# Optimization experiments

Hardware: AMD Instinct MI355X
Metric: run time of the kernel (lower is better)

Reference implementation:

```python
import jax, jax.numpy as jnp
import numpy as np

B, L, D = 2, 2048, 1024
H, G = 16, 2            # num_heads, num_kv_groups
HPG = H // G            # heads per kv group = 8
DQK, DV = 128, 128      # qk_head_dim, v_head_dim (head_dim=64, ratios=2.0)


def setup_inputs() -> dict:
    key = jax.random.key(0)
    ks = jax.random.split(key, 12)

    def xavier(k, shape, scale=1.0):
        fan_in, fan_out = shape[0], shape[1]
        lim = np.sqrt(6.0 / (fan_in + fan_out))
        return jax.random.uniform(k, shape, jnp.float32, -lim, lim) * scale

    return {
        "in_q": jax.random.normal(ks[0], (B, L, D), jnp.float32),
        "in_k": jax.random.normal(ks[1], (B, L, D), jnp.float32),
        "in_v": jax.random.normal(ks[2], (B, L, D), jnp.float32),
        # weights stored as [in, out] (transpose of torch Linear); qk_init_scale=0.5
        "Wq": xavier(ks[3], (D, H * DQK), 0.5),
        "bq": jnp.zeros((H * DQK,), jnp.float32),
        "Wk": xavier(ks[4], (D, G * DQK), 0.5),
        "bk": jnp.zeros((G * DQK,), jnp.float32),
        "Wv": xavier(ks[5], (D, G * DV)),
        "bv": jnp.zeros((G * DV,), jnp.float32),
        "Wo": xavier(ks[6], (H * DV, D)),
        "bo": jnp.zeros((D,), jnp.float32),
        "q_extra_scale": jnp.ones((1,), jnp.float32),
    }


def reference(in_q, in_k, in_v, Wq, bq, Wk, bk, Wv, bv, Wo, bo, q_extra_scale):
    # fused projections
    q = (in_q @ Wq + bq) * q_extra_scale              # [B,L,H*DQK]
    k = in_k @ Wk + bk                                 # [B,L,G*DQK]
    v = in_v @ Wv + bv                                 # [B,L,G*DV]

    # reshape: keep GQA group structure instead of materializing repeat_interleave
    q = q.reshape(B, L, G, HPG, DQK)                   # heads grouped: head h = g*HPG + m
    k = k.reshape(B, L, G, DQK)
    v = v.reshape(B, L, G, DV)

    scale = 1.0 / np.sqrt(DQK)
    # scores: [B,G,HPG,L_q,L_kv]
    scores = jnp.einsum("bsgmd,btgd->bgmst", q, k) * scale
    causal = jnp.tril(jnp.ones((L, L), bool))          # is_causal=True
    scores = jnp.where(causal, scores, jnp.finfo(scores.dtype).min)
    attn = jax.nn.softmax(scores, axis=-1)
    ctx = jnp.einsum("bgmst,btgd->bsgmd", attn, v)     # [B,L,G,HPG,DV]
    ctx = ctx.reshape(B, L, H * DV)
    return ctx @ Wo + bo                               # [B,L,D]
```

## Files before the change

kernel.cpp:

```cpp
#include <hip/hip_runtime.h>


typedef __bf16 bf16;
typedef __bf16 bf16x8 __attribute__((ext_vector_type(8)));
typedef __bf16 bf16x4 __attribute__((ext_vector_type(4)));
typedef float f32x4 __attribute__((ext_vector_type(4)));
typedef float float4v __attribute__((ext_vector_type(4)));

#define MFMA_BF16(a, b, c) __builtin_amdgcn_mfma_f32_16x16x32_bf16((a), (b), (c), 0, 0, 0)

static constexpr int Bz = 2, Lz = 2048, Dz = 1024;
static constexpr int Hz = 16, Gz = 2;
static constexpr int DQKz = 128, DVz = 128;

__device__ __forceinline__ void async_copy16(const bf16* g, bf16* l) {
    __builtin_amdgcn_global_load_lds(
        (const __attribute__((address_space(1))) unsigned int*)g,
        (__attribute__((address_space(3))) unsigned int*)l, 16, 0, 0);
}

__global__ __launch_bounds__(256) void prep(
    const float* __restrict__ q, const float* __restrict__ k,
    const float* __restrict__ v, bf16* __restrict__ dq,
    bf16* __restrict__ dk, bf16* __restrict__ dv,
    const float* __restrict__ Wq, const float* __restrict__ Wk,
    const float* __restrict__ Wv, const float* __restrict__ Wo,
    bf16* __restrict__ WqT, bf16* __restrict__ WkT,
    bf16* __restrict__ WvT, bf16* __restrict__ WoT)
{
    int bid = blockIdx.x;
    if (bid < 6144) {
        const float* s = bid < 2048 ? q : (bid < 4096 ? k : v);
        bf16* d = bid < 2048 ? dq : (bid < 4096 ? dk : dv);
        int i = (bid & 2047) * 2048 + threadIdx.x * 8;
        float4v a = *(const float4v*)(s + i);
        float4v b = *(const float4v*)(s + i + 4);
        bf16x8 o;
        #pragma unroll
        for (int j = 0; j < 4; ++j) { o[j] = (bf16)a[j]; o[j + 4] = (bf16)b[j]; }
        *(bf16x8*)(d + i) = o;
        return;
    }
    bid -= 6144;
    const float* W; bf16* WT; int K, N;
    if (bid < 2048)      { W = Wq; WT = WqT; K = 1024; N = 2048; }
    else if (bid < 2304) { W = Wk; WT = WkT; K = 1024; N = 256;  bid -= 2048; }
    else if (bid < 2560) { W = Wv; WT = WvT; K = 1024; N = 256;  bid -= 2304; }
    else                 { W = Wo; WT = WoT; K = 2048; N = 1024; bid -= 2560; }
    int tiles_n = N >> 5;
    int n0 = (bid % tiles_n) * 32, k0 = (bid / tiles_n) * 32;

    __shared__ bf16 t[32][33];
    int tx = threadIdx.x & 31, ty = threadIdx.x >> 5;
    #pragma unroll
    for (int i = 0; i < 4; ++i)
        t[ty + i * 8][tx] = (bf16)W[(size_t)(k0 + ty + i * 8) * N + n0 + tx];
    __syncthreads();
    #pragma unroll
    for (int i = 0; i < 4; ++i)
        WT[(size_t)(n0 + ty + i * 8) * K + k0 + tx] = t[tx][ty + i * 8];
}

template <typename TC>
__device__ __forceinline__ void gemm_tile(
    const bf16* __restrict__ A, const bf16* __restrict__ BT,
    const float* __restrict__ bias, float scale, TC* __restrict__ C,
    int M, int N, int K, int m0, int n0, bool trans_out,
    bf16 (&As)[2][128 * 64], bf16 (&Bs)[2][128 * 64])
{
    const int tid  = threadIdx.x;
    const int wave = tid >> 6;
    const int lane = tid & 63;
    const int quad = lane >> 4;
    const int l16  = lane & 15;
    const int sw   = l16 & 7;
    const int wm = wave >> 2, wn = wave & 3;

    f32x4 acc[4][2] = {};

    auto stage = [&](int k0, int buf) {
        #pragma unroll
        for (int s = 0; s < 2; ++s) {
            int i = s * 512 + tid;
            int row = i >> 3, c = (i & 7) ^ (row & 7);
            async_copy16(A + (size_t)(m0 + row) * K + k0 + c * 8, &As[buf][i * 8]);
        }
        #pragma unroll
        for (int s = 0; s < 2; ++s) {
            int i = s * 512 + tid;
            int row = i >> 3, c = (i & 7) ^ (row & 7);
            async_copy16(BT + (size_t)(n0 + row) * K + k0 + c * 8, &Bs[buf][i * 8]);
        }
    };

    stage(0, 0);
    int cur = 0;
    for (int k0 = 0; k0 < K; k0 += 64) {
        __syncthreads();
        if (k0 + 64 < K) stage(k0 + 64, cur ^ 1);

        #pragma unroll
        for (int ks = 0; ks < 2; ++ks) {
            bf16x8 af[4], bfv[2];
            #pragma unroll
            for (int mt = 0; mt < 4; ++mt)
                af[mt] = *(const bf16x8*)(&As[cur][((wm * 64 + mt * 16 + l16) * 8
                                                    + ((ks * 4 + quad) ^ sw)) * 8]);
            #pragma unroll
            for (int nt = 0; nt < 2; ++nt)
                bfv[nt] = *(const bf16x8*)(&Bs[cur][((wn * 32 + nt * 16 + l16) * 8
                                                     + ((ks * 4 + quad) ^ sw)) * 8]);
            #pragma unroll
            for (int mt = 0; mt < 4; ++mt)
                #pragma unroll
                for (int nt = 0; nt < 2; ++nt)
                    acc[mt][nt] = MFMA_BF16(af[mt], bfv[nt], acc[mt][nt]);
        }
        cur ^= 1;
    }

    #pragma unroll
    for (int nt = 0; nt < 2; ++nt) {
        int col = n0 + wn * 32 + nt * 16 + l16;
        float bv = bias[col];
        #pragma unroll
        for (int mt = 0; mt < 4; ++mt) {
            int row = m0 + wm * 64 + mt * 16 + quad * 4;
            if (trans_out) {
                struct V4 { TC v[4]; } o;
                #pragma unroll
                for (int r = 0; r < 4; ++r)
                    o.v[r] = (TC)((acc[mt][nt][r] + bv) * scale);
                *(V4*)(&C[(size_t)col * M + row]) = o;
            } else {
                #pragma unroll
                for (int r = 0; r < 4; ++r)
                    C[(size_t)(row + r) * N + col] =
                        (TC)((acc[mt][nt][r] + bv) * scale);
            }
        }
    }
}

__global__ __launch_bounds__(512, 4) void proj_qkv(
    const bf16* __restrict__ aq, const bf16* __restrict__ ak,
    const bf16* __restrict__ av, const bf16* __restrict__ WqT,
    const bf16* __restrict__ WkT, const bf16* __restrict__ WvT,
    const float* __restrict__ bq, const float* __restrict__ bk,
    const float* __restrict__ bv, const float* __restrict__ qsc,
    bf16* __restrict__ Qw, bf16* __restrict__ Kw, bf16* __restrict__ VwT)
{
    __shared__ bf16 As[2][128 * 64];
    __shared__ bf16 Bs[2][128 * 64];
    int bid = blockIdx.x;
    if (bid < 512) {
        float scale = qsc[0] * 0.08838834764831845f * 1.4426950408889634f;
        gemm_tile<bf16>(aq, WqT, bq, scale, Qw, 4096, 2048, 1024,
                        (bid >> 4) * 128, (bid & 15) * 128, false, As, Bs);
    } else if (bid < 576) {
        int b2 = bid - 512;
        gemm_tile<bf16>(ak, WkT, bk, 1.0f, Kw, 4096, 256, 1024,
                        (b2 >> 1) * 128, (b2 & 1) * 128, false, As, Bs);
    } else {
        int b2 = bid - 576;
        gemm_tile<bf16>(av, WvT, bv, 1.0f, VwT, 4096, 256, 1024,
                        (b2 >> 1) * 128, (b2 & 1) * 128, true, As, Bs);
    }
}

__global__ __launch_bounds__(512, 4) void proj_o(
    const bf16* __restrict__ Cw, const bf16* __restrict__ WoT,
    const float* __restrict__ bo, float* __restrict__ out)
{
    __shared__ bf16 As[2][128 * 64];
    __shared__ bf16 Bs[2][128 * 64];
    gemm_tile<float>(Cw, WoT, bo, 1.0f, out, 4096, 1024, 2048,
                     (blockIdx.x >> 3) * 128, (blockIdx.x & 7) * 128,
                     false, As, Bs);
}

__global__ __launch_bounds__(256, 2) void attn_fused(
    const bf16* __restrict__ Q,
    const bf16* __restrict__ Kp,
    const bf16* __restrict__ VT,
    bf16* __restrict__ ctx)
{
    __shared__ bf16 Kb[2][64 * 128];
    __shared__ bf16 Vb[2][128 * 64];
    __shared__ bf16 Ps[4][16 * 72];

    const int tid  = threadIdx.x;
    const int wave = tid >> 6;
    const int lane = tid & 63;
    const int quad = lane >> 4;
    const int l16  = lane & 15;
    const int sw   = l16 & 7;

    const int h = blockIdx.y;
    const int b = blockIdx.z;
    const int g = h >> 3;

    const bf16* kgbase = Kp + (size_t)(b * Lz) * (Gz * DQKz) + g * DQKz;
    const bf16* vgbase = VT + (size_t)(g * DVz) * (Bz * Lz) + b * Lz;

    auto stage = [&](int kt, int buf) {
        const bf16* kb = kgbase + (size_t)(kt * 64) * (Gz * DQKz);
        #pragma unroll
        for (int s = 0; s < 4; ++s) {
            int i = s * 256 + tid;
            int key = i >> 4, c = (i & 15) ^ (key & 7);
            async_copy16(kb + (size_t)key * (Gz * DQKz) + c * 8, &Kb[buf][i * 8]);
        }
        const bf16* vb = vgbase + kt * 64;
        #pragma unroll
        for (int s = 0; s < 4; ++s) {
            int i = s * 256 + tid;
            int dv = i >> 3, c = (i & 7) ^ (dv & 7);
            async_copy16(vb + (size_t)dv * (Bz * Lz) + c * 8, &Vb[buf][i * 8]);
        }
    };

    for (int pass = 0; pass < 2; ++pass) {
        const int qt  = pass == 0 ? (31 - blockIdx.x) : blockIdx.x;
        const int q0  = qt * 64;
        const int nkt = qt + 1;
        const int qrow = q0 + wave * 16 + l16;

        bf16x8 qf[4];
        {
            const bf16* qbase = Q + (size_t)(b * Lz + qrow) * (Hz * DQKz) + h * DQKz;
            #pragma unroll
            for (int ks = 0; ks < 4; ++ks)
                qf[ks] = *(const bf16x8*)(qbase + ks * 32 + quad * 8);
        }

        f32x4 oacc[8] = {};
        float lsum = 0.0f;

        if (pass) __syncthreads();
        stage(0, 0);
        int cur = 0;

        bf16* ps = Ps[wave];

        for (int kt = 0; kt < nkt; ++kt) {
            __syncthreads();
            if (kt + 1 < nkt) stage(kt + 1, cur ^ 1);

            const bf16* kcur = Kb[cur];
            const bf16* vcur = Vb[cur];

            f32x4 sacc[4] = {};
            #pragma unroll
            for (int nf = 0; nf < 4; ++nf) {
                #pragma unroll
                for (int ks = 0; ks < 4; ++ks) {
                    bf16x8 kf = *(const bf16x8*)(&kcur[((nf * 16 + l16) * 16
                                                        + ((ks * 4 + quad) ^ sw)) * 8]);
                    sacc[nf] = MFMA_BF16(kf, qf[ks], sacc[nf]);
                }
            }

            float pv[4][4];
            if (kt == nkt - 1) {
                const int kv0 = kt * 64;
                #pragma unroll
                for (int nf = 0; nf < 4; ++nf) {
                    int keyb = kv0 + nf * 16 + quad * 4;
                    #pragma unroll
                    for (int r = 0; r < 4; ++r)
                        pv[nf][r] = (keyb + r > qrow) ? 0.0f
                                                      : exp2f(sacc[nf][r] - 8.0f);
                }
            } else {
                #pragma unroll
                for (int nf = 0; nf < 4; ++nf)
                    #pragma unroll
                    for (int r = 0; r < 4; ++r)
                        pv[nf][r] = exp2f(sacc[nf][r] - 8.0f);
            }

            #pragma unroll
            for (int nf = 0; nf < 4; ++nf)
                lsum += (pv[nf][0] + pv[nf][1]) + (pv[nf][2] + pv[nf][3]);

            #pragma unroll
            for (int nf = 0; nf < 4; ++nf) {
                bf16x4 pk;
                #pragma unroll
                for (int r = 0; r < 4; ++r) pk[r] = (bf16)pv[nf][r];
                *(bf16x4*)(&ps[l16 * 72 + nf * 16 + quad * 4]) = pk;
            }

            #pragma unroll
            for (int ks2 = 0; ks2 < 2; ++ks2) {
                bf16x8 pf = *(const bf16x8*)(&ps[l16 * 72 + ks2 * 32 + quad * 8]);
                #pragma unroll
                for (int nf2 = 0; nf2 < 8; ++nf2) {
                    bf16x8 vf = *(const bf16x8*)(&vcur[((nf2 * 16 + l16) * 8
                                                        + ((ks2 * 4 + quad) ^ sw)) * 8]);
                    oacc[nf2] = MFMA_BF16(vf, pf, oacc[nf2]);
                }
            }
            cur ^= 1;
        }

        lsum += __shfl_xor(lsum, 16);
        lsum += __shfl_xor(lsum, 32);
        const float inv = 1.0f / lsum;

        bf16* cbase = ctx + (size_t)(b * Lz + qrow) * (Hz * DVz) + h * DVz;
        #pragma unroll
        for (int nf2 = 0; nf2 < 8; ++nf2) {
            bf16x4 o4;
            #pragma unroll
            for (int r = 0; r < 4; ++r) o4[r] = (bf16)(oacc[nf2][r] * inv);
            *(bf16x4*)(&cbase[nf2 * 16 + quad * 4]) = o4;
        }
    }
}

extern "C" void kernel_launch(void* const* d_in, const int* in_sizes, int n_in,
                              void* d_out, int out_size, void* d_ws, size_t ws_size,
                              hipStream_t stream)
{
    (void)in_sizes; (void)n_in; (void)out_size; (void)ws_size;

    const float* in_q = (const float*)d_in[0];
    const float* in_k = (const float*)d_in[1];
    const float* in_v = (const float*)d_in[2];
    const float* Wq   = (const float*)d_in[3];
    const float* bq   = (const float*)d_in[4];
    const float* Wk   = (const float*)d_in[5];
    const float* bk   = (const float*)d_in[6];
    const float* Wv   = (const float*)d_in[7];
    const float* bv   = (const float*)d_in[8];
    const float* Wo   = (const float*)d_in[9];
    const float* bo   = (const float*)d_in[10];
    const float* qsc  = (const float*)d_in[11];
    float* out = (float*)d_out;

    const int M = Bz * Lz;
    const int NQ = Hz * DQKz;
    const int NKV = Gz * DQKz;

    bf16* aq  = (bf16*)d_ws;
    bf16* WqT = aq  + (size_t)M * Dz;
    bf16* WkT = WqT + (size_t)NQ * Dz;
    bf16* WvT = WkT + (size_t)NKV * Dz;
    bf16* WoT = WvT + (size_t)NKV * Dz;
    bf16* Qw  = WoT + (size_t)Dz * NQ;
    bf16* Kw  = Qw  + (size_t)M * NQ;
    bf16* VwT = Kw  + (size_t)M * NKV;
    bf16* Cw  = VwT + (size_t)NKV * M;
    bf16* ak  = Cw;
    bf16* av  = Cw + (size_t)M * Dz;

    prep<<<dim3(10752), dim3(256), 0, stream>>>(
        in_q, in_k, in_v, aq, ak, av, Wq, Wk, Wv, Wo, WqT, WkT, WvT, WoT);

    proj_qkv<<<dim3(640), dim3(512), 0, stream>>>(
        aq, ak, av, WqT, WkT, WvT, bq, bk, bv, qsc, Qw, Kw, VwT);

    attn_fused<<<dim3(Lz / 128, Hz, Bz), dim3(256), 0, stream>>>(Qw, Kw, VwT, Cw);

    proj_o<<<dim3(256), dim3(512), 0, stream>>>(Cw, WoT, bo, out);
}
```

Measured before the change: 263.7 us.

## Switch attention to 32x32 MFMA with split-KV waves and register-resident P

Rewrites the attention inner loop to use 32x32x16 bf16 MFMAs, with waves split as 2 query tiles by 2 KV halves. The softmax probabilities are packed with v_cvt_pk_bf16 and rearranged via permlane32_swap, so they stay in registers instead of round-tripping through LDS. The two KV-half partial outputs and row sums are combined through LDS at the end of each pass. Staging and fragment offsets are also precomputed outside the loop, trading extra epilogue synchronisation and register pressure for fewer LDS operations and larger MFMA tiles.

```diff
diff --git a/kernel.cpp b/kernel.cpp
--- a/kernel.cpp
+++ b/kernel.cpp
@@ -5,9 +5,11 @@
 typedef __bf16 bf16x8 __attribute__((ext_vector_type(8)));
 typedef __bf16 bf16x4 __attribute__((ext_vector_type(4)));
 typedef float f32x4 __attribute__((ext_vector_type(4)));
+typedef float f32x16 __attribute__((ext_vector_type(16)));
 typedef float float4v __attribute__((ext_vector_type(4)));
 
 #define MFMA_BF16(a, b, c) __builtin_amdgcn_mfma_f32_16x16x32_bf16((a), (b), (c), 0, 0, 0)
+#define MFMA32(a, b, c)    __builtin_amdgcn_mfma_f32_32x32x16_bf16((a), (b), (c), 0, 0, 0)
 
 static constexpr int Bz = 2, Lz = 2048, Dz = 1024;
 static constexpr int Hz = 16, Gz = 2;
@@ -17,6 +19,12 @@
     __builtin_amdgcn_global_load_lds(
         (const __attribute__((address_space(1))) unsigned int*)g,
         (__attribute__((address_space(3))) unsigned int*)l, 16, 0, 0);
+}
+
+__device__ __forceinline__ unsigned cvt_pk_bf16(float lo, float hi) {
+    unsigned r;
+    asm("v_cvt_pk_bf16_f32 %0, %1, %2" : "=v"(r) : "v"(lo), "v"(hi));
+    return r;
 }
 
 __global__ __launch_bounds__(256) void prep(
@@ -187,14 +195,15 @@
 {
     __shared__ bf16 Kb[2][64 * 128];
     __shared__ bf16 Vb[2][128 * 64];
-    __shared__ bf16 Ps[4][16 * 72];
 
     const int tid  = threadIdx.x;
     const int wave = tid >> 6;
     const int lane = tid & 63;
-    const int quad = lane >> 4;
-    const int l16  = lane & 15;
-    const int sw   = l16 & 7;
+    const int hi   = lane >> 5;
+    const int l31  = lane & 31;
+    const int s7   = l31 & 7;
+    const int wq   = wave >> 1;
+    const int kvw  = wave & 1;
 
     const int h = blockIdx.y;
     const int b = blockIdx.z;
@@ -203,46 +212,58 @@
     const bf16* kgbase = Kp + (size_t)(b * Lz) * (Gz * DQKz) + g * DQKz;
     const bf16* vgbase = VT + (size_t)(g * DVz) * (Bz * Lz) + b * Lz;
 
+    int kgo[4], vgo[4], ldso[4];
+    #pragma unroll
+    for (int s = 0; s < 4; ++s) {
+        int i = s * 256 + tid;
+        ldso[s] = i * 8;
+        int key = i >> 4, ck = (i & 15) ^ (key & 7);
+        kgo[s] = key * (Gz * DQKz) + ck * 8;
+        int dvr = i >> 3, cv = (i & 7) ^ (dvr & 7);
+        vgo[s] = dvr * (Bz * Lz) + cv * 8;
+    }
     auto stage = [&](int kt, int buf) {
         const bf16* kb = kgbase + (size_t)(kt * 64) * (Gz * DQKz);
-        #pragma unroll
-        for (int s = 0; s < 4; ++s) {
-            int i = s * 256 + tid;
-            int key = i >> 4, c = (i & 15) ^ (key & 7);
-            async_copy16(kb + (size_t)key * (Gz * DQKz) + c * 8, &Kb[buf][i * 8]);
-        }
         const bf16* vb = vgbase + kt * 64;
         #pragma unroll
-        for (int s = 0; s < 4; ++s) {
-            int i = s * 256 + tid;
-            int dv = i >> 3, c = (i & 7) ^ (dv & 7);
-            async_copy16(vb + (size_t)dv * (Bz * Lz) + c * 8, &Vb[buf][i * 8]);
-        }
+        for (int s = 0; s < 4; ++s) async_copy16(kb + kgo[s], &Kb[buf][ldso[s]]);
+        #pragma unroll
+        for (int s = 0; s < 4; ++s) async_copy16(vb + vgo[s], &Vb[buf][ldso[s]]);
     };
 
+    int koff[8];
+    #pragma unroll
+    for (int ks = 0; ks < 8; ++ks)
+        koff[ks] = ((kvw * 32 + l31) * 16 + ((ks * 2 + hi) ^ s7)) * 8;
+    int voff[4][2];
+    #pragma unroll
+    for (int dt = 0; dt < 4; ++dt)
+        #pragma unroll
+        for (int kss = 0; kss < 2; ++kss)
+            voff[dt][kss] = ((dt * 32 + l31) * 8
+                             + ((kvw * 4 + kss * 2 + hi) ^ s7)) * 8;
+
     for (int pass = 0; pass < 2; ++pass) {
-        const int qt  = pass == 0 ? (31 - blockIdx.x) : blockIdx.x;
+        const int qt  = pass == 0 ? (31 - (int)blockIdx.x) : (int)blockIdx.x;
         const int q0  = qt * 64;
         const int nkt = qt + 1;
-        const int qrow = q0 + wave * 16 + l16;
-
-        bf16x8 qf[4];
+        const int qrow = q0 + wq * 32 + l31;
+
+        bf16x8 qf[8];
         {
             const bf16* qbase = Q + (size_t)(b * Lz + qrow) * (Hz * DQKz) + h * DQKz;
             #pragma unroll
-            for (int ks = 0; ks < 4; ++ks)
-                qf[ks] = *(const bf16x8*)(qbase + ks * 32 + quad * 8);
-        }
-
-        f32x4 oacc[8] = {};
+            for (int s = 0; s < 8; ++s)
+                qf[s] = *(const bf16x8*)(qbase + s * 16 + hi * 8);
+        }
+
+        f32x16 oacc[4] = {};
         float lsum = 0.0f;
 
         if (pass) __syncthreads();
         stage(0, 0);
         int cur = 0;
 
-        bf16* ps = Ps[wave];
-
         for (int kt = 0; kt < nkt; ++kt) {
             __syncthreads();
             if (kt + 1 < nkt) stage(kt + 1, cur ^ 1);
@@ -250,72 +271,92 @@
             const bf16* kcur = Kb[cur];
             const bf16* vcur = Vb[cur];
 
-            f32x4 sacc[4] = {};
-            #pragma unroll
-            for (int nf = 0; nf < 4; ++nf) {
-                #pragma unroll
-                for (int ks = 0; ks < 4; ++ks) {
-                    bf16x8 kf = *(const bf16x8*)(&kcur[((nf * 16 + l16) * 16
-                                                        + ((ks * 4 + quad) ^ sw)) * 8]);
-                    sacc[nf] = MFMA_BF16(kf, qf[ks], sacc[nf]);
-                }
-            }
-
-            float pv[4][4];
+            f32x16 sacc = {};
+            #pragma unroll
+            for (int ks = 0; ks < 8; ++ks) {
+                bf16x8 kf = *(const bf16x8*)(kcur + koff[ks]);
+                sacc = MFMA32(kf, qf[ks], sacc);
+            }
+
+            float pv[16];
             if (kt == nkt - 1) {
-                const int kv0 = kt * 64;
-                #pragma unroll
-                for (int nf = 0; nf < 4; ++nf) {
-                    int keyb = kv0 + nf * 16 + quad * 4;
-                    #pragma unroll
-                    for (int r = 0; r < 4; ++r)
-                        pv[nf][r] = (keyb + r > qrow) ? 0.0f
-                                                      : exp2f(sacc[nf][r] - 8.0f);
+                #pragma unroll
+                for (int r = 0; r < 16; ++r) {
+                    int key = kvw * 32 + (r & 3) + 8 * (r >> 2) + 4 * hi;
+                    pv[r] = (key > wq * 32 + l31) ? 0.0f
+                                                  : exp2f(sacc[r] - 8.0f);
                 }
             } else {
                 #pragma unroll
-                for (int nf = 0; nf < 4; ++nf)
-                    #pragma unroll
-                    for (int r = 0; r < 4; ++r)
-                        pv[nf][r] = exp2f(sacc[nf][r] - 8.0f);
-            }
-
-            #pragma unroll
-            for (int nf = 0; nf < 4; ++nf)
-                lsum += (pv[nf][0] + pv[nf][1]) + (pv[nf][2] + pv[nf][3]);
-
-            #pragma unroll
-            for (int nf = 0; nf < 4; ++nf) {
-                bf16x4 pk;
-                #pragma unroll
-                for (int r = 0; r < 4; ++r) pk[r] = (bf16)pv[nf][r];
-                *(bf16x4*)(&ps[l16 * 72 + nf * 16 + quad * 4]) = pk;
-            }
-
-            #pragma unroll
-            for (int ks2 = 0; ks2 < 2; ++ks2) {
-                bf16x8 pf = *(const bf16x8*)(&ps[l16 * 72 + ks2 * 32 + quad * 8]);
-                #pragma unroll
-                for (int nf2 = 0; nf2 < 8; ++nf2) {
-                    bf16x8 vf = *(const bf16x8*)(&vcur[((nf2 * 16 + l16) * 8
-                                                        + ((ks2 * 4 + quad) ^ sw)) * 8]);
-                    oacc[nf2] = MFMA_BF16(vf, pf, oacc[nf2]);
-                }
+                for (int r = 0; r < 16; ++r)
+                    pv[r] = exp2f(sacc[r] - 8.0f);
+            }
+            lsum += ((pv[0] + pv[1]) + (pv[2] + pv[3]))
+                  + ((pv[4] + pv[5]) + (pv[6] + pv[7]))
+                  + ((pv[8] + pv[9]) + (pv[10] + pv[11]))
+                  + ((pv[12] + pv[13]) + (pv[14] + pv[15]));
+
+            unsigned c0 = cvt_pk_bf16(pv[0],  pv[1]);
+            unsigned c1 = cvt_pk_bf16(pv[2],  pv[3]);
+            unsigned c2 = cvt_pk_bf16(pv[4],  pv[5]);
+            unsigned c3 = cvt_pk_bf16(pv[6],  pv[7]);
+            unsigned c4 = cvt_pk_bf16(pv[8],  pv[9]);
+            unsigned c5 = cvt_pk_bf16(pv[10], pv[11]);
+            unsigned c6 = cvt_pk_bf16(pv[12], pv[13]);
+            unsigned c7 = cvt_pk_bf16(pv[14], pv[15]);
+            asm("v_permlane32_swap_b32 %0, %1" : "+v"(c0), "+v"(c2));
+            asm("v_permlane32_swap_b32 %0, %1" : "+v"(c1), "+v"(c3));
+            asm("v_permlane32_swap_b32 %0, %1" : "+v"(c4), "+v"(c6));
+            asm("v_permlane32_swap_b32 %0, %1" : "+v"(c5), "+v"(c7));
+            union { unsigned u[4]; bf16x8 v; } p0 = {{c0, c1, c2, c3}};
+            union { unsigned u[4]; bf16x8 v; } p1 = {{c4, c5, c6, c7}};
+
+            #pragma unroll
+            for (int dt = 0; dt < 4; ++dt) {
+                bf16x8 vf0 = *(const bf16x8*)(vcur + voff[dt][0]);
+                oacc[dt] = MFMA32(vf0, p0.v, oacc[dt]);
+                bf16x8 vf1 = *(const bf16x8*)(vcur + voff[dt][1]);
+                oacc[dt] = MFMA32(vf1, p1.v, oacc[dt]);
             }
             cur ^= 1;
         }
 
-        lsum += __shfl_xor(lsum, 16);
         lsum += __shfl_xor(lsum, 32);
+
+        float* E0 = (float*)Kb;
+        float* E1 = (float*)Vb;
+        float* LS = (float*)Vb + 6000;
+        __syncthreads();
+        #pragma unroll
+        for (int t = 0; t < 2; ++t) {
+            int dt = (1 - kvw) * 2 + t;
+            float* E = t ? E1 : E0;
+            #pragma unroll
+            for (int j = 0; j < 4; ++j) {
+                f32x4 v4 = { oacc[dt][4 * j],     oacc[dt][4 * j + 1],
+                             oacc[dt][4 * j + 2], oacc[dt][4 * j + 3] };
+                *(f32x4*)&E[(wave * 64 + lane) * 20 + 4 * j] = v4;
+            }
+        }
+        if (lane < 32) LS[wave * 32 + lane] = lsum;
+        __syncthreads();
+        lsum += LS[(wave ^ 1) * 32 + l31];
         const float inv = 1.0f / lsum;
 
         bf16* cbase = ctx + (size_t)(b * Lz + qrow) * (Hz * DVz) + h * DVz;
         #pragma unroll
-        for (int nf2 = 0; nf2 < 8; ++nf2) {
-            bf16x4 o4;
-            #pragma unroll
-            for (int r = 0; r < 4; ++r) o4[r] = (bf16)(oacc[nf2][r] * inv);
-            *(bf16x4*)(&cbase[nf2 * 16 + quad * 4]) = o4;
+        for (int t = 0; t < 2; ++t) {
+            int dt = kvw * 2 + t;
+            float* E = t ? E1 : E0;
+            #pragma unroll
+            for (int j = 0; j < 4; ++j) {
+                f32x4 p4 = *(const f32x4*)&E[((wave ^ 1) * 64 + lane) * 20 + 4 * j];
+                bf16x4 o4;
+                #pragma unroll
+                for (int r = 0; r < 4; ++r)
+                    o4[r] = (bf16)((oacc[dt][4 * j + r] + p4[r]) * inv);
+                *(bf16x4*)&cbase[dt * 32 + j * 8 + hi * 4] = o4;
+            }
         }
     }
 }
```

Result: slower. 476.5 us (+80.7%).
